# Kernel tuning notes

Hardware: AMD Instinct MI355X
Metric: run time of the kernel (lower is better)

Reference implementation:

```python
import jax, jax.numpy as jnp
import numpy as np

LENGTH_OF_SIGNAL = 2560
OUTLIER_THRESHOLD = 3.0


def setup_inputs() -> dict:
    key = jax.random.key(0)
    inputs = jax.random.normal(key, (16384, 2560, 1), dtype=jnp.float32)
    return {"inputs": inputs}


def reference(inputs):
    # inputs: (B, S, 1). All stats reduce over the sequence axis (dim=1).
    B, S, _ = inputs.shape
    x = inputs[..., 0]  # (B, S)

    mean = jnp.mean(x, axis=1)                       # (B,)
    maximum = jnp.max(x, axis=1)
    minimum = jnp.min(x, axis=1)
    p2p = maximum - minimum
    rms = jnp.sqrt(jnp.mean(x * x, axis=1))
    var = jnp.var(x, axis=1, ddof=1)                 # torch.var is unbiased
    std = jnp.sqrt(var)                              # torch.std is unbiased

    centered = x - mean[:, None]
    skewness = jnp.mean(centered ** 3, axis=1) / (std ** 3)
    kurtosis = jnp.mean(centered ** 4, axis=1) / (std ** 4)

    abs_x = jnp.abs(x)
    abs_sum = jnp.sum(abs_x, axis=1)
    abs_max = jnp.max(abs_x, axis=1)
    shape_factor = rms * LENGTH_OF_SIGNAL / abs_sum
    impulse_factor = abs_max * LENGTH_OF_SIGNAL / abs_sum

    outliers = jnp.sum(
        (jnp.abs(centered) > OUTLIER_THRESHOLD * std[:, None]).astype(jnp.int32),
        axis=1,
    ).astype(jnp.float32)

    # zero-crossing rate on flattened (B, S) signal
    zcr = jnp.sum(
        (jnp.diff(jnp.sign(x), axis=1) != 0).astype(jnp.float32), axis=1
    ) / (2.0 * S)

    # Hjorth parameters (activity, mobility, complexity)
    d1 = jnp.diff(x, axis=1)
    d2 = jnp.diff(d1, axis=1)
    var_d1 = jnp.var(d1, axis=1, ddof=1)
    var_d2 = jnp.var(d2, axis=1, ddof=1)
    activity = var
    mobility = jnp.sqrt(var_d1 / var)
    complexity = jnp.sqrt(var_d2 / var_d1)

    stacked = jnp.stack(
        [mean, maximum, minimum, p2p, var, rms, skewness, kurtosis,
         shape_factor, impulse_factor, outliers, zcr,
         activity, mobility, complexity],
        axis=1,
    )  # (B, 15)
    return stacked
```

## Files before the change

### kernel.cpp

```cpp
#include <hip/hip_runtime.h>
#include <math.h>


typedef float f32x2 __attribute__((ext_vector_type(2)));
typedef float f32x4 __attribute__((ext_vector_type(4)));

constexpr int S_LEN = 2560;

#define DPP_ADD_F32(x, ctrl) do { \
    int t_ = __builtin_amdgcn_update_dpp(0, __float_as_int(x), ctrl, 0xf, 0xf, false); \
    x += __int_as_float(t_); } while (0)
#define DPP_MAX_F32(x, ctrl) do { \
    int t_ = __builtin_amdgcn_update_dpp(__float_as_int(x), __float_as_int(x), ctrl, 0xf, 0xf, false); \
    x = fmaxf(x, __int_as_float(t_)); } while (0)
#define DPP_MIN_F32(x, ctrl) do { \
    int t_ = __builtin_amdgcn_update_dpp(__float_as_int(x), __float_as_int(x), ctrl, 0xf, 0xf, false); \
    x = fminf(x, __int_as_float(t_)); } while (0)

__device__ __forceinline__ float wave_sum_f32(float x) {
    DPP_ADD_F32(x, 0x111); DPP_ADD_F32(x, 0x112); DPP_ADD_F32(x, 0x114);
    DPP_ADD_F32(x, 0x118); DPP_ADD_F32(x, 0x142); DPP_ADD_F32(x, 0x143);
    return x;
}
__device__ __forceinline__ float wave_max_f32(float x) {
    DPP_MAX_F32(x, 0x111); DPP_MAX_F32(x, 0x112); DPP_MAX_F32(x, 0x114);
    DPP_MAX_F32(x, 0x118); DPP_MAX_F32(x, 0x142); DPP_MAX_F32(x, 0x143);
    return x;
}
__device__ __forceinline__ float wave_min_f32(float x) {
    DPP_MIN_F32(x, 0x111); DPP_MIN_F32(x, 0x112); DPP_MIN_F32(x, 0x114);
    DPP_MIN_F32(x, 0x118); DPP_MIN_F32(x, 0x142); DPP_MIN_F32(x, 0x143);
    return x;
}
__device__ __forceinline__ double wave_sum_f64(double x) {
#define DPP_ADD_F64(ctrl) do { \
    long long b_ = __double_as_longlong(x); \
    int lo_ = __builtin_amdgcn_update_dpp(0, (int)(b_ & 0xffffffffLL), ctrl, 0xf, 0xf, false); \
    int hi_ = __builtin_amdgcn_update_dpp(0, (int)(b_ >> 32), ctrl, 0xf, 0xf, false); \
    x += __longlong_as_double(((long long)hi_ << 32) | (unsigned int)lo_); } while (0)
    DPP_ADD_F64(0x111); DPP_ADD_F64(0x112); DPP_ADD_F64(0x114);
    DPP_ADD_F64(0x118); DPP_ADD_F64(0x142); DPP_ADD_F64(0x143);
#undef DPP_ADD_F64
    return x;
}
__device__ __forceinline__ double readlane_f64(double x, int l) {
    long long b = __double_as_longlong(x);
    int lo = __builtin_amdgcn_readlane((int)(b & 0xffffffffLL), l);
    int hi = __builtin_amdgcn_readlane((int)(b >> 32), l);
    return __longlong_as_double(((long long)hi << 32) | (unsigned int)lo);
}

__global__ __launch_bounds__(256, 6)
void health_stats(const float* __restrict__ in, float* __restrict__ out) {
    const int lane = threadIdx.x & 63;
    const int wid  = threadIdx.x >> 6;
    const int row  = blockIdx.x * 4 + wid;

    const f32x4* rp = reinterpret_cast<const f32x4*>(in)
                    + (size_t)row * (S_LEN / 4) + lane;

    f32x4 X[10];
#pragma unroll
    for (int k = 0; k < 10; ++k) X[k] = rp[k * 64];

    const float ep0 = __int_as_float(__builtin_amdgcn_readlane(__float_as_int(X[0][0]), 0));
    const float ep1 = __int_as_float(__builtin_amdgcn_readlane(__float_as_int(X[0][1]), 0));

    f32x2 sp = {0.f, 0.f}, qp = {0.f, 0.f}, sabsp = {0.f, 0.f};
    f32x2 vmaxp = {-INFINITY, -INFINITY}, vminp = {INFINITY, INFINITY};
#pragma unroll
    for (int k = 0; k < 10; ++k) {
        f32x2 lo = __builtin_shufflevector(X[k], X[k], 0, 1);
        f32x2 hi = __builtin_shufflevector(X[k], X[k], 2, 3);
        sp += lo + hi;
        qp = __builtin_elementwise_fma(lo, lo, qp);
        qp = __builtin_elementwise_fma(hi, hi, qp);
        sabsp += __builtin_elementwise_max(lo, -lo);
        sabsp += __builtin_elementwise_max(hi, -hi);
        vmaxp = __builtin_elementwise_max(vmaxp, __builtin_elementwise_max(lo, hi));
        vminp = __builtin_elementwise_min(vminp, __builtin_elementwise_min(lo, hi));
    }

    const double sum_l = (double)sp.x + (double)sp.y;
    const double sq_l  = (double)qp.x + (double)qp.y;
    const double tsum = readlane_f64(wave_sum_f64(sum_l), 63);
    const double tsq  = readlane_f64(wave_sum_f64(sq_l), 63);

    float sabs_t = wave_sum_f32(sabsp.x + sabsp.y);
    float vmax_t = wave_max_f32(fmaxf(vmaxp.x, vmaxp.y));
    float vmin_t = wave_min_f32(fminf(vminp.x, vminp.y));

    const double mean = tsum * (1.0 / S_LEN);
    const double var  = (tsq - tsum * mean) * (1.0 / (S_LEN - 1));
    const double stdv = sqrt(var);
    const double thr  = 3.0 * stdv;

    const double bhi = mean + thr, blo = mean - thr;
    float bhi_f = (float)bhi;
    if ((double)bhi_f > bhi) bhi_f = __int_as_float(__float_as_int(bhi_f) - 1);
    float blo_f = (float)blo;
    if ((double)blo_f < blo) blo_f = __int_as_float(__float_as_int(blo_f) - 1);

    const float mf = (float)mean;
    const f32x2 nmf2 = {-mf, -mf};
    const int nli = (lane + 1) & 63;

    f32x2 c3p = {0.f, 0.f}, c4p = {0.f, 0.f};
    float r1 = 0.f, r2 = 0.f;
    int outc = 0, zcc = 0;

#pragma unroll
    for (int k = 0; k < 10; ++k) {
        const float x0 = X[k][0], x1 = X[k][1], x2v = X[k][2], x3 = X[k][3];
        float v0, v1;
        if (k < 9) {
            v0 = (lane == 0) ? X[k + 1][0] : x0;
            v1 = (lane == 0) ? X[k + 1][1] : x1;
        } else {
            v0 = (lane == 0) ? 0.f : x0;
            v1 = (lane == 0) ? 0.f : x1;
        }
        const float n0 = __shfl(v0, nli);
        const float n1 = __shfl(v1, nli);

        f32x2 lo = __builtin_shufflevector(X[k], X[k], 0, 1);
        f32x2 hi = __builtin_shufflevector(X[k], X[k], 2, 3);
        f32x2 cl = lo + nmf2, ch = hi + nmf2;
        f32x2 ql = cl * cl,  qh = ch * ch;
        c3p = __builtin_elementwise_fma(ql, cl, c3p);
        c3p = __builtin_elementwise_fma(qh, ch, c3p);
        c4p = __builtin_elementwise_fma(ql, ql, c4p);
        c4p = __builtin_elementwise_fma(qh, qh, c4p);

        outc += __popcll(__ballot(x0  > bhi_f || x0  < blo_f));
        outc += __popcll(__ballot(x1  > bhi_f || x1  < blo_f));
        outc += __popcll(__ballot(x2v > bhi_f || x2v < blo_f));
        outc += __popcll(__ballot(x3  > bhi_f || x3  < blo_f));

        const unsigned long long m0 = __ballot(x0  < 0.f);
        const unsigned long long m1 = __ballot(x1  < 0.f);
        const unsigned long long m2 = __ballot(x2v < 0.f);
        const unsigned long long m3 = __ballot(x3  < 0.f);
        const unsigned long long mn = __ballot(n0  < 0.f);
        zcc += __popcll(m0 ^ m1) + __popcll(m1 ^ m2) + __popcll(m2 ^ m3);
        zcc += __popcll((m3 ^ mn) & ((k == 9) ? 0x7FFFFFFFFFFFFFFFULL : ~0ULL));

        r1 = fmaf(x0, x1, fmaf(x1, x2v, fmaf(x2v, x3, fmaf(x3, n0, r1))));
        r2 = fmaf(x0, x2v, fmaf(x1, x3, fmaf(x2v, n0, fmaf(x3, n1, r2))));
    }

    const float c3_t = wave_sum_f32(c3p.x + c3p.y);
    const float c4_t = wave_sum_f32(c4p.x + c4p.y);
    const float r1_t = wave_sum_f32(r1);
    const float r2_t = wave_sum_f32(r2);

    if (lane == 63) {
        const double rms  = sqrt(tsq * (1.0 / S_LEN));
        const double m3d  = (double)c3_t * (1.0 / S_LEN);
        const double m4d  = (double)c4_t * (1.0 / S_LEN);
        const double skew = m3d / (var * stdv);
        const double kurt = m4d / (var * var);
        const float  amax = fmaxf(fabsf(vmax_t), fabsf(vmin_t));
        const double shape   = rms * (double)S_LEN / (double)sabs_t;
        const double impulse = (double)amax * (double)S_LEN / (double)sabs_t;

        const double e0 = (double)ep0, e1 = (double)ep1;
        const double e2 = (double)X[9][2], e3 = (double)X[9][3];
        const double Q = tsq, r1d = (double)r1_t, r2d = (double)r2_t;
        const double s1q = 2.0 * Q - 2.0 * r1d - e0 * e0 - e3 * e3;
        const double s2q = 6.0 * Q - 8.0 * r1d + 2.0 * r2d
                         + 4.0 * (e0 * e1 + e2 * e3)
                         - 5.0 * e0 * e0 - e1 * e1 - e2 * e2 - 5.0 * e3 * e3;
        const double sd1 = e3 - e0;
        const double sd2 = (e3 - e2) - (e1 - e0);
        const double var1 = (s1q - sd1 * sd1 * (1.0 / (S_LEN - 1))) * (1.0 / (S_LEN - 2));
        const double var2 = (s2q - sd2 * sd2 * (1.0 / (S_LEN - 2))) * (1.0 / (S_LEN - 3));

        float* o = out + (size_t)row * 15;
        o[0]  = (float)mean;
        o[1]  = vmax_t;
        o[2]  = vmin_t;
        o[3]  = vmax_t - vmin_t;
        o[4]  = (float)var;
        o[5]  = (float)rms;
        o[6]  = (float)skew;
        o[7]  = (float)kurt;
        o[8]  = (float)shape;
        o[9]  = (float)impulse;
        o[10] = (float)outc;
        o[11] = (float)zcc * (1.0f / (2.0f * S_LEN));
        o[12] = (float)var;
        o[13] = (float)sqrt(var1 / var);
        o[14] = (float)sqrt(var2 / var1);
    }
}

extern "C" void kernel_launch(void* const* d_in, const int* in_sizes, int n_in,
                              void* d_out, int out_size, void* d_ws, size_t ws_size,
                              hipStream_t stream) {
    (void)in_sizes; (void)n_in; (void)d_ws; (void)ws_size; (void)out_size;
    const float* in = (const float*)d_in[0];
    float* out = (float*)d_out;
    health_stats<<<4096, 256, 0, stream>>>(in, out);
}
```

Baseline: 41.07 us.

## Split each row across two waves and combine partials via shared memory

Each row is now handled by two wavefronts, each covering half of the sequence, with the grid doubled to 8192 blocks. Partial sums, extrema, moments, neighbour boundary values and counts are exchanged through LDS with two block barriers, and one wave writes the final outputs. This halves the registers each wave holds for its slice of the row and exposes more memory-level parallelism per CU, at the cost of LDS traffic, two __syncthreads per block and double rounding in the cross-wave combine.

```diff
diff --git a/kernel.cpp b/kernel.cpp
--- a/kernel.cpp
+++ b/kernel.cpp
@@ -50,26 +50,34 @@
     return __longlong_as_double(((long long)hi << 32) | (unsigned int)lo);
 }
 
+struct RowShared {
+    double sum[2], sq[2];
+    float  nb0, nb1;
+    float  h1v[11];
+};
+
 __global__ __launch_bounds__(256, 6)
 void health_stats(const float* __restrict__ in, float* __restrict__ out) {
+    __shared__ RowShared RS[2];
+
     const int lane = threadIdx.x & 63;
     const int wid  = threadIdx.x >> 6;
-    const int row  = blockIdx.x * 4 + wid;
+    const int hidx = wid & 1;
+    const int rsl  = wid >> 1;
+    const int row  = blockIdx.x * 2 + rsl;
+    RowShared& R = RS[rsl];
 
     const f32x4* rp = reinterpret_cast<const f32x4*>(in)
-                    + (size_t)row * (S_LEN / 4) + lane;
-
-    f32x4 X[10];
+                    + (size_t)row * (S_LEN / 4) + hidx * (1280 / 4) + lane;
+
+    f32x4 X[5];
 #pragma unroll
-    for (int k = 0; k < 10; ++k) X[k] = rp[k * 64];
-
-    const float ep0 = __int_as_float(__builtin_amdgcn_readlane(__float_as_int(X[0][0]), 0));
-    const float ep1 = __int_as_float(__builtin_amdgcn_readlane(__float_as_int(X[0][1]), 0));
+    for (int k = 0; k < 5; ++k) X[k] = rp[k * 64];
 
     f32x2 sp = {0.f, 0.f}, qp = {0.f, 0.f}, sabsp = {0.f, 0.f};
     f32x2 vmaxp = {-INFINITY, -INFINITY}, vminp = {INFINITY, INFINITY};
 #pragma unroll
-    for (int k = 0; k < 10; ++k) {
+    for (int k = 0; k < 5; ++k) {
         f32x2 lo = __builtin_shufflevector(X[k], X[k], 0, 1);
         f32x2 hi = __builtin_shufflevector(X[k], X[k], 2, 3);
         sp += lo + hi;
@@ -83,17 +91,24 @@
 
     const double sum_l = (double)sp.x + (double)sp.y;
     const double sq_l  = (double)qp.x + (double)qp.y;
-    const double tsum = readlane_f64(wave_sum_f64(sum_l), 63);
-    const double tsq  = readlane_f64(wave_sum_f64(sq_l), 63);
+    const double sum_u = readlane_f64(wave_sum_f64(sum_l), 63);
+    const double sq_u  = readlane_f64(wave_sum_f64(sq_l), 63);
 
     float sabs_t = wave_sum_f32(sabsp.x + sabsp.y);
     float vmax_t = wave_max_f32(fmaxf(vmaxp.x, vmaxp.y));
     float vmin_t = wave_min_f32(fminf(vminp.x, vminp.y));
 
+    if (lane == 0) {
+        R.sum[hidx] = sum_u;  R.sq[hidx] = sq_u;
+        if (hidx == 1) { R.nb0 = X[0][0]; R.nb1 = X[0][1]; }
+    }
+    __syncthreads();
+    const double tsum = R.sum[0] + R.sum[1];
+    const double tsq  = R.sq[0]  + R.sq[1];
+
     const double mean = tsum * (1.0 / S_LEN);
     const double var  = (tsq - tsum * mean) * (1.0 / (S_LEN - 1));
-    const double stdv = sqrt(var);
-    const double thr  = 3.0 * stdv;
+    const double thr  = 3.0 * sqrt(var);
 
     const double bhi = mean + thr, blo = mean - thr;
     float bhi_f = (float)bhi;
@@ -101,27 +116,26 @@
     float blo_f = (float)blo;
     if ((double)blo_f < blo) blo_f = __int_as_float(__float_as_int(blo_f) - 1);
 
+    const float nbv0 = (hidx == 0) ? R.nb0 : 0.f;
+    const float nbv1 = (hidx == 0) ? R.nb1 : 0.f;
     const float mf = (float)mean;
     const f32x2 nmf2 = {-mf, -mf};
     const int nli = (lane + 1) & 63;
+    const unsigned long long tail_ok = (hidx == 0) ? ~0ULL : 0x7FFFFFFFFFFFFFFFULL;
 
     f32x2 c3p = {0.f, 0.f}, c4p = {0.f, 0.f};
     float r1 = 0.f, r2 = 0.f;
     int outc = 0, zcc = 0;
 
 #pragma unroll
-    for (int k = 0; k < 10; ++k) {
+    for (int k = 0; k < 5; ++k) {
         const float x0 = X[k][0], x1 = X[k][1], x2v = X[k][2], x3 = X[k][3];
-        float v0, v1;
-        if (k < 9) {
-            v0 = (lane == 0) ? X[k + 1][0] : x0;
-            v1 = (lane == 0) ? X[k + 1][1] : x1;
-        } else {
-            v0 = (lane == 0) ? 0.f : x0;
-            v1 = (lane == 0) ? 0.f : x1;
-        }
-        const float n0 = __shfl(v0, nli);
-        const float n1 = __shfl(v1, nli);
+        const int kn = (k == 4) ? 0 : (k + 1);
+        float v0 = (lane == 0) ? X[kn][0] : x0;
+        float v1 = (lane == 0) ? X[kn][1] : x1;
+        float n0 = __shfl(v0, nli);
+        float n1 = __shfl(v1, nli);
+        if (k == 4 && lane == 63) { n0 = nbv0; n1 = nbv1; }
 
         f32x2 lo = __builtin_shufflevector(X[k], X[k], 0, 1);
         f32x2 hi = __builtin_shufflevector(X[k], X[k], 2, 3);
@@ -143,7 +157,7 @@
         const unsigned long long m3 = __ballot(x3  < 0.f);
         const unsigned long long mn = __ballot(n0  < 0.f);
         zcc += __popcll(m0 ^ m1) + __popcll(m1 ^ m2) + __popcll(m2 ^ m3);
-        zcc += __popcll((m3 ^ mn) & ((k == 9) ? 0x7FFFFFFFFFFFFFFFULL : ~0ULL));
+        zcc += __popcll((m3 ^ mn) & ((k == 4) ? tail_ok : ~0ULL));
 
         r1 = fmaf(x0, x1, fmaf(x1, x2v, fmaf(x2v, x3, fmaf(x3, n0, r1))));
         r2 = fmaf(x0, x2v, fmaf(x1, x3, fmaf(x2v, n0, fmaf(x3, n1, r2))));
@@ -154,19 +168,42 @@
     const float r1_t = wave_sum_f32(r1);
     const float r2_t = wave_sum_f32(r2);
 
-    if (lane == 63) {
+    if (hidx == 1 && lane == 63) {
+        R.h1v[0] = sabs_t; R.h1v[1] = vmax_t; R.h1v[2] = vmin_t;
+        R.h1v[3] = c3_t;   R.h1v[4] = c4_t;
+        R.h1v[5] = r1_t;   R.h1v[6] = r2_t;
+        R.h1v[7] = (float)outc; R.h1v[8] = (float)zcc;
+        R.h1v[9] = X[4][2]; R.h1v[10] = X[4][3];
+    }
+    const float ep0 = __int_as_float(__builtin_amdgcn_readlane(__float_as_int(X[0][0]), 0));
+    const float ep1 = __int_as_float(__builtin_amdgcn_readlane(__float_as_int(X[0][1]), 0));
+
+    __syncthreads();
+
+    if (hidx == 0 && lane == 63) {
+        const float tabs = sabs_t + R.h1v[0];
+        const float tmax = fmaxf(vmax_t, R.h1v[1]);
+        const float tmin = fminf(vmin_t, R.h1v[2]);
+        const float c3f  = c3_t + R.h1v[3];
+        const float c4f  = c4_t + R.h1v[4];
+        const double r1d = (double)r1_t + (double)R.h1v[5];
+        const double r2d = (double)r2_t + (double)R.h1v[6];
+        const float outt = (float)outc + R.h1v[7];
+        const float zct  = (float)zcc + R.h1v[8];
+        const double e2 = (double)R.h1v[9], e3 = (double)R.h1v[10];
+        const double e0 = (double)ep0, e1 = (double)ep1;
+
+        const double stdv = sqrt(var);
         const double rms  = sqrt(tsq * (1.0 / S_LEN));
-        const double m3d  = (double)c3_t * (1.0 / S_LEN);
-        const double m4d  = (double)c4_t * (1.0 / S_LEN);
+        const double m3d  = (double)c3f * (1.0 / S_LEN);
+        const double m4d  = (double)c4f * (1.0 / S_LEN);
         const double skew = m3d / (var * stdv);
         const double kurt = m4d / (var * var);
-        const float  amax = fmaxf(fabsf(vmax_t), fabsf(vmin_t));
-        const double shape   = rms * (double)S_LEN / (double)sabs_t;
-        const double impulse = (double)amax * (double)S_LEN / (double)sabs_t;
-
-        const double e0 = (double)ep0, e1 = (double)ep1;
-        const double e2 = (double)X[9][2], e3 = (double)X[9][3];
-        const double Q = tsq, r1d = (double)r1_t, r2d = (double)r2_t;
+        const float  amax = fmaxf(fabsf(tmax), fabsf(tmin));
+        const double shape   = rms * (double)S_LEN / (double)tabs;
+        const double impulse = (double)amax * (double)S_LEN / (double)tabs;
+
+        const double Q = tsq;
         const double s1q = 2.0 * Q - 2.0 * r1d - e0 * e0 - e3 * e3;
         const double s2q = 6.0 * Q - 8.0 * r1d + 2.0 * r2d
                          + 4.0 * (e0 * e1 + e2 * e3)
@@ -178,17 +215,17 @@
 
         float* o = out + (size_t)row * 15;
         o[0]  = (float)mean;
-        o[1]  = vmax_t;
-        o[2]  = vmin_t;
-        o[3]  = vmax_t - vmin_t;
+        o[1]  = tmax;
+        o[2]  = tmin;
+        o[3]  = tmax - tmin;
         o[4]  = (float)var;
         o[5]  = (float)rms;
         o[6]  = (float)skew;
         o[7]  = (float)kurt;
         o[8]  = (float)shape;
         o[9]  = (float)impulse;
-        o[10] = (float)outc;
-        o[11] = (float)zcc * (1.0f / (2.0f * S_LEN));
+        o[10] = outt;
+        o[11] = zct * (1.0f / (2.0f * S_LEN));
         o[12] = (float)var;
         o[13] = (float)sqrt(var1 / var);
         o[14] = (float)sqrt(var2 / var1);
@@ -201,5 +238,5 @@
     (void)in_sizes; (void)n_in; (void)d_ws; (void)ws_size; (void)out_size;
     const float* in = (const float*)d_in[0];
     float* out = (float*)d_out;
-    health_stats<<<4096, 256, 0, stream>>>(in, out);
-}
+    health_stats<<<8192, 256, 0, stream>>>(in, out);
+}
```

Result: slower. 43.30 us (+5.4%).
